# Performance work log

Hardware: AMD Instinct MI355X
Metric: run time of the kernel (lower is better)

The kernel has to match this reference:

```python
import jax, jax.numpy as jnp
import numpy as np

B, T, C = 128, 512, 512
EPS = 1e-5


def setup_inputs() -> dict:
    key = jax.random.key(0)
    ks = jax.random.split(key, 12)
    s_tri = 1.0 / np.sqrt(T)   # rough torch Linear init scale (per-row fan-in varies; fixed for simplicity)
    s_fc1 = 1.0 / np.sqrt(C)
    s_fc2 = 1.0 / np.sqrt(2 * C)
    return {
        "inputs": jax.random.normal(ks[0], (B, T, C), dtype=jnp.float32),
        "ln1_w": jnp.ones((T, C), jnp.float32),
        "ln1_b": jnp.zeros((T, C), jnp.float32),
        "ln2_w": jnp.ones((T, C), jnp.float32),
        "ln2_b": jnp.zeros((T, C), jnp.float32),
        # Row s of triu_W corresponds to nn.Linear(s+1, 1); entries j> s are masked in reference().
        "triu_W": jax.random.uniform(ks[1], (T, T), jnp.float32, -s_tri, s_tri),
        "triu_b": jax.random.uniform(ks[2], (T,), jnp.float32, -s_tri, s_tri),
        "fc1_W": jax.random.uniform(ks[3], (2 * C, C), jnp.float32, -s_fc1, s_fc1),
        "fc1_b": jax.random.uniform(ks[4], (2 * C,), jnp.float32, -s_fc1, s_fc1),
        "fc2_W": jax.random.uniform(ks[5], (C, 2 * C), jnp.float32, -s_fc2, s_fc2),
        "fc2_b": jax.random.uniform(ks[6], (C,), jnp.float32, -s_fc2, s_fc2),
    }


def _layernorm_2d(x, w, b):
    # torch nn.LayerNorm((T, C)): normalize jointly over the last TWO dims.
    mu = jnp.mean(x, axis=(-2, -1), keepdims=True)
    var = jnp.var(x, axis=(-2, -1), keepdims=True)
    return (x - mu) * jax.lax.rsqrt(var + EPS) * w + b


def reference(inputs, ln1_w, ln1_b, ln2_w, ln2_b, triu_W, triu_b, fc1_W, fc1_b, fc2_W, fc2_b):
    x = _layernorm_2d(inputs, ln1_w, ln1_b)                       # [B,T,C]
    # TriU time mixer on x.mT ([B,C,T]): out[..., s] = sum_{t<=s} W[s,t]*x[..., t] + b[s]
    Wm = jnp.tril(triu_W)                                          # causal mask
    xm = jnp.einsum('btc,st->bsc', x, Wm) + triu_b[None, :, None]  # [B,T,C] (already back-transposed)
    x2 = _layernorm_2d(xm + inputs, ln2_w, ln2_b)                  # [B,T,C]
    h = jax.nn.gelu(jnp.einsum('btc,hc->bth', x2, fc1_W) + fc1_b, approximate=False)
    y = jnp.einsum('bth,ch->btc', h, fc2_W) + fc2_b
    return x2 + y
```

## Files before the change

### kernel.cpp

```cpp
#include <hip/hip_runtime.h>
#include <cstdint>

typedef unsigned short u16;
typedef __attribute__((ext_vector_type(8))) short s16x8;
typedef __attribute__((ext_vector_type(4))) float f32x4;
typedef __attribute__((ext_vector_type(8))) unsigned short u16x8;
typedef __attribute__((ext_vector_type(4))) unsigned short u16x4;

#define B_ 128
#define T_ 512
#define C_ 512
#define TC 262144

static __device__ __forceinline__ float bf2f(u16 u) {
  union { unsigned int i; float f; } v; v.i = ((unsigned int)u) << 16; return v.f;
}
static __device__ __forceinline__ u16 f2bf(float f) {
  union { float fv; unsigned int i; } v; v.fv = f;
  unsigned int r = (v.i + 0x7FFFu + ((v.i >> 16) & 1u)) >> 16;
  return (u16)r;
}

static __device__ __forceinline__ float gelu_tanh(float x) {
  float z = 0.7978845608028654f * (x + 0.044715f * x * x * x);
  float e = __expf(2.0f * z);
  float t = 1.0f - 2.0f / (e + 1.0f);
  return 0.5f * x * (1.0f + t);
}

#define GLD16(gp, lp) __builtin_amdgcn_global_load_lds( \
    (const __attribute__((address_space(1))) void*)(gp), \
    (__attribute__((address_space(3))) void*)(lp), 16, 0, 0)


__global__ __launch_bounds__(256)
void reduce_stats_kernel(const float* __restrict__ X, float2* __restrict__ partials) {
  const int b = blockIdx.y, blk = blockIdx.x, tid = threadIdx.x;
  const float* p = X + (size_t)b * TC + (size_t)blk * 2048 + (size_t)tid * 8;
  f32x4 v0 = *(const f32x4*)p;
  f32x4 v1 = *(const f32x4*)(p + 4);
  float s = 0.f, q = 0.f;
#pragma unroll
  for (int i = 0; i < 4; ++i) { s += v0[i] + v1[i]; q += v0[i] * v0[i] + v1[i] * v1[i]; }
  for (int o = 32; o; o >>= 1) { s += __shfl_down(s, o); q += __shfl_down(q, o); }
  __shared__ float ss[4], qq[4];
  if ((tid & 63) == 0) { ss[tid >> 6] = s; qq[tid >> 6] = q; }
  __syncthreads();
  if (tid == 0)
    partials[(size_t)b * 128 + blk] =
        make_float2(ss[0] + ss[1] + ss[2] + ss[3], qq[0] + qq[1] + qq[2] + qq[3]);
}

__global__ __launch_bounds__(128)
void finalize_stats_kernel(const float2* __restrict__ partials, float2* __restrict__ stats) {
  const int b = blockIdx.x, tid = threadIdx.x;
  float2 v = partials[(size_t)b * 128 + tid];
  float s = v.x, q = v.y;
  for (int o = 32; o; o >>= 1) { s += __shfl_down(s, o); q += __shfl_down(q, o); }
  __shared__ float ss[2], qq[2];
  if ((tid & 63) == 0) { ss[tid >> 6] = s; qq[tid >> 6] = q; }
  __syncthreads();
  if (tid == 0) {
    float sm = ss[0] + ss[1], sq = qq[0] + qq[1];
    float mean = sm * (1.f / (float)TC);
    float var = sq * (1.f / (float)TC) - mean * mean;
    stats[b] = make_float2(mean, rsqrtf(var + 1e-5f));
  }
}

__global__ __launch_bounds__(64)
void finalize_stats16_kernel(const float2* __restrict__ partials, float2* __restrict__ stats) {
  const int b = blockIdx.x, tid = threadIdx.x;
  float s = 0.f, q = 0.f;
  if (tid < 16) { float2 v = partials[(size_t)b * 16 + tid]; s = v.x; q = v.y; }
  for (int o = 32; o; o >>= 1) { s += __shfl_down(s, o); q += __shfl_down(q, o); }
  if (tid == 0) {
    float mean = s * (1.f / (float)TC);
    float var = q * (1.f / (float)TC) - mean * mean;
    stats[b] = make_float2(mean, rsqrtf(var + 1e-5f));
  }
}


__global__ __launch_bounds__(256)
void ln1_transpose_kernel(const float* __restrict__ X, const float* __restrict__ W,
                          const float* __restrict__ Bv, const float2* __restrict__ stats,
                          u16* __restrict__ xT) {
  const int b = blockIdx.z;
  const int t0 = blockIdx.y * 64, c0 = blockIdx.x * 64;
  const float2 st = stats[b];
  const float mu = st.x, rs = st.y;
  __shared__ u16 tile[64][72];
  const int tid = threadIdx.x;
  const int rr = tid >> 4;
  const int cc = (tid & 15) * 4;
#pragma unroll
  for (int i = 0; i < 4; ++i) {
    const int lt = i * 16 + rr;
    const size_t wi = (size_t)(t0 + lt) * C_ + c0 + cc;
    f32x4 x = *(const f32x4*)(X + (size_t)b * TC + wi);
    f32x4 w = *(const f32x4*)(W + wi);
    f32x4 bb = *(const f32x4*)(Bv + wi);
#pragma unroll
    for (int j = 0; j < 4; ++j)
      tile[lt][cc + j] = f2bf((x[j] - mu) * rs * w[j] + bb[j]);
  }
  __syncthreads();
  const int c = tid >> 2;
  const int tg = (tid & 3) * 16;
  u16 buf[16];
#pragma unroll
  for (int i = 0; i < 16; ++i) buf[i] = tile[tg + i][c];
  const size_t o = (size_t)b * TC + (size_t)(c0 + c) * T_ + t0 + tg;
  u16x8 o0, o1;
#pragma unroll
  for (int i = 0; i < 8; ++i) { o0[i] = buf[i]; o1[i] = buf[8 + i]; }
  *(u16x8*)(xT + o) = o0;
  *(u16x8*)(xT + o + 8) = o1;
}


__global__ __launch_bounds__(256)
void ln2_apply_kernel(const u16* __restrict__ S, const float* __restrict__ W,
                      const float* __restrict__ Bv, const float2* __restrict__ stats,
                      u16* __restrict__ x2) {
  const size_t i = ((size_t)blockIdx.x * 256 + threadIdx.x) * 8;
  const int b = (int)(i >> 18);
  const size_t r = i & (size_t)(TC - 1);
  const float2 st = stats[b];
  const float mu = st.x, rs = st.y;
  u16x8 sv = *(const u16x8*)(S + i);
  f32x4 w0 = *(const f32x4*)(W + r);
  f32x4 w1 = *(const f32x4*)(W + r + 4);
  f32x4 b0 = *(const f32x4*)(Bv + r);
  f32x4 b1 = *(const f32x4*)(Bv + r + 4);
  u16x8 o;
#pragma unroll
  for (int j = 0; j < 4; ++j) {
    o[j]     = f2bf((bf2f(sv[j])     - mu) * rs * w0[j] + b0[j]);
    o[4 + j] = f2bf((bf2f(sv[4 + j]) - mu) * rs * w1[j] + b1[j]);
  }
  *(u16x8*)(x2 + i) = o;
}


__global__ __launch_bounds__(256)
void cvt_bf16_kernel(const float* __restrict__ X, u16* __restrict__ Y) {
  const size_t i = ((size_t)blockIdx.x * 256 + threadIdx.x) * 4;
  f32x4 v = *(const f32x4*)(X + i);
  u16x4 o;
#pragma unroll
  for (int j = 0; j < 4; ++j) o[j] = f2bf(v[j]);
  *(u16x4*)(Y + i) = o;
}

__global__ __launch_bounds__(256)
void tril_bf16_kernel(const float* __restrict__ Wt, u16* __restrict__ Y) {
  const int i = blockIdx.x * 256 + threadIdx.x;
  const int s = i >> 9, t = i & 511;
  Y[i] = f2bf(t <= s ? Wt[i] : 0.f);
}


template <int MODE>
__global__ __launch_bounds__(256)
void gemm_bt_kernel(const u16* __restrict__ A, const u16* __restrict__ Bm,
                    int K, int lda, int ldb,
                    void* __restrict__ Cp, int ldc,
                    const float* __restrict__ bias,
                    const void* __restrict__ res,
                    long long strideB, long long strideC,
                    float2* __restrict__ stat_part) {
  __shared__ u16 As[2][128 * 32];
  __shared__ u16 Bs[2][128 * 32];
  const int tid = threadIdx.x;

  const int nwg = gridDim.x;
  const int orig = blockIdx.x;
  const int swz = (orig & 7) * (nwg >> 3) + (orig >> 3);
  int bx, by, bz;
  if (MODE == 0) { bz = swz >> 4; by = (swz >> 2) & 3; bx = swz & 3; }
  else if (MODE == 1) { bz = 0; by = swz >> 3; bx = swz & 7; }
  else { bz = 0; by = swz >> 2; bx = swz & 3; }

  const u16* Bp = Bm + (size_t)bz * (size_t)strideB;
  const int m0 = by * 128, n0 = bx * 128;
  int kTiles = K >> 5;
  if (MODE == 0) { const int need = (by + 1) * 4; if (need < kTiles) kTiles = need; }

  const int lane = tid & 63;
  const int wave = tid >> 6;
  const int wm = (wave >> 1) * 64;
  const int wn = (wave & 1) * 64;
  const int lr = lane & 15;
  const int kg = lane >> 4;

  const int srow = tid >> 2;
  const int ske = (tid & 3) * 8;

  f32x4 acc[4][4];
  const f32x4 zero = {0.f, 0.f, 0.f, 0.f};
#pragma unroll
  for (int m = 0; m < 4; ++m)
#pragma unroll
    for (int n = 0; n < 4; ++n) acc[m][n] = zero;

  auto STAGE = [&](int buf, int kt) {
    const int k0 = kt << 5;
#pragma unroll
    for (int i = 0; i < 2; ++i) {
      const int row = i * 64 + srow;
      const int c = i * 256 + tid;
      GLD16(A + (size_t)(m0 + row) * lda + k0 + ske, &As[buf][c * 8]);
      GLD16(Bp + (size_t)(n0 + row) * ldb + k0 + ske, &Bs[buf][c * 8]);
    }
  };

  STAGE(0, 0);
  int cur = 0;
  for (int kt = 0; kt < kTiles; ++kt) {
    __syncthreads();
    if (kt + 1 < kTiles) STAGE(cur ^ 1, kt + 1);
    s16x8 af[4], bf[4];
#pragma unroll
    for (int m = 0; m < 4; ++m) af[m] = *(const s16x8*)&As[cur][(wm + m * 16 + lr) * 32 + kg * 8];
#pragma unroll
    for (int n = 0; n < 4; ++n) bf[n] = *(const s16x8*)&Bs[cur][(wn + n * 16 + lr) * 32 + kg * 8];
#pragma unroll
    for (int m = 0; m < 4; ++m)
#pragma unroll
      for (int n = 0; n < 4; ++n)
        acc[m][n] = __builtin_amdgcn_mfma_f32_16x16x32_bf16(af[m], bf[n], acc[m][n], 0, 0, 0);
    cur ^= 1;
  }

  if (MODE == 0) {
    u16* Cptr = (u16*)Cp + (size_t)bz * (size_t)strideC;
    const float* inp = (const float*)res + (size_t)bz * (size_t)strideC;
    float psum = 0.f, psq = 0.f;
#pragma unroll
    for (int m = 0; m < 4; ++m) {
      const int rb = m0 + wm + m * 16 + kg * 4;
#pragma unroll
      for (int n = 0; n < 4; ++n) {
        const int col = n0 + wn + n * 16 + lr;
#pragma unroll
        for (int j = 0; j < 4; ++j) {
          const size_t idx = (size_t)(rb + j) * ldc + col;
          float v = acc[m][n][j] + inp[idx] + bias[rb + j];
          psum += v; psq += v * v;
          Cptr[idx] = f2bf(v);
        }
      }
    }
    for (int o = 32; o; o >>= 1) { psum += __shfl_down(psum, o); psq += __shfl_down(psq, o); }
    __shared__ float rs_[4], rq_[4];
    if (lane == 0) { rs_[wave] = psum; rq_[wave] = psq; }
    __syncthreads();
    if (tid == 0)
      stat_part[(size_t)bz * 16 + by * 4 + bx] =
          make_float2(rs_[0] + rs_[1] + rs_[2] + rs_[3], rq_[0] + rq_[1] + rq_[2] + rq_[3]);
  } else if (MODE == 1) {
    u16* Cptr = (u16*)Cp;
#pragma unroll
    for (int m = 0; m < 4; ++m) {
      const int rb = m0 + wm + m * 16 + kg * 4;
#pragma unroll
      for (int n = 0; n < 4; ++n) {
        const int col = n0 + wn + n * 16 + lr;
        const float bs = bias[col];
#pragma unroll
        for (int j = 0; j < 4; ++j) {
          float v = acc[m][n][j] + bs;
          Cptr[(size_t)(rb + j) * ldc + col] = f2bf(gelu_tanh(v));
        }
      }
    }
  } else {
    float* Cptr = (float*)Cp;
    const u16* x2p = (const u16*)res;
#pragma unroll
    for (int m = 0; m < 4; ++m) {
      const int rb = m0 + wm + m * 16 + kg * 4;
#pragma unroll
      for (int n = 0; n < 4; ++n) {
        const int col = n0 + wn + n * 16 + lr;
        const float bs = bias[col];
#pragma unroll
        for (int j = 0; j < 4; ++j) {
          const size_t idx = (size_t)(rb + j) * ldc + col;
          Cptr[idx] = acc[m][n][j] + bs + bf2f(x2p[idx]);
        }
      }
    }
  }
}


extern "C" void kernel_launch(void* const* d_in, const int* in_sizes, int n_in,
                              void* d_out, int out_size, void* d_ws, size_t ws_size,
                              hipStream_t stream) {
  const float* inputs = (const float*)d_in[0];
  const float* ln1_w  = (const float*)d_in[1];
  const float* ln1_b  = (const float*)d_in[2];
  const float* ln2_w  = (const float*)d_in[3];
  const float* ln2_b  = (const float*)d_in[4];
  const float* triu_W = (const float*)d_in[5];
  const float* triu_b = (const float*)d_in[6];
  const float* fc1_W  = (const float*)d_in[7];
  const float* fc1_b  = (const float*)d_in[8];
  const float* fc2_W  = (const float*)d_in[9];
  const float* fc2_b  = (const float*)d_in[10];
  float* out = (float*)d_out;
  (void)in_sizes; (void)n_in; (void)out_size; (void)ws_size;

  char* ws = (char*)d_ws;
  size_t off = 0;
  auto carve = [&](size_t bytes) {
    char* p = ws + off;
    off += (bytes + 255) & ~(size_t)255;
    return p;
  };
  u16* s_bf = (u16*)carve((size_t)B_ * T_ * C_ * 2);
  u16* xT   = (u16*)carve((size_t)B_ * T_ * C_ * 2);
  u16* x2   = xT;
  u16* h    = (u16*)carve((size_t)B_ * T_ * 2 * C_ * 2);
  u16* wmb  = (u16*)carve((size_t)T_ * T_ * 2);
  u16* w1b  = (u16*)carve((size_t)2 * C_ * C_ * 2);
  u16* w2b  = (u16*)carve((size_t)C_ * 2 * C_ * 2);
  float2* partials  = (float2*)carve(128 * 128 * sizeof(float2));
  float2* partials2 = (float2*)carve(128 * 16 * sizeof(float2));
  float2* stats1 = (float2*)carve(128 * sizeof(float2));
  float2* stats2 = (float2*)carve(128 * sizeof(float2));

  reduce_stats_kernel<<<dim3(128, 128), 256, 0, stream>>>(inputs, partials);
  finalize_stats_kernel<<<128, 128, 0, stream>>>(partials, stats1);
  ln1_transpose_kernel<<<dim3(8, 8, 128), 256, 0, stream>>>(inputs, ln1_w, ln1_b, stats1, xT);
  tril_bf16_kernel<<<1024, 256, 0, stream>>>(triu_W, wmb);
  cvt_bf16_kernel<<<512, 256, 0, stream>>>(fc1_W, w1b);
  cvt_bf16_kernel<<<512, 256, 0, stream>>>(fc2_W, w2b);
  gemm_bt_kernel<0><<<2048, 256, 0, stream>>>(
      wmb, xT, 512, 512, 512, s_bf, 512, triu_b, inputs, (long long)TC, (long long)TC, partials2);
  finalize_stats16_kernel<<<128, 64, 0, stream>>>(partials2, stats2);
  ln2_apply_kernel<<<16384, 256, 0, stream>>>(s_bf, ln2_w, ln2_b, stats2, x2);
  gemm_bt_kernel<1><<<4096, 256, 0, stream>>>(
      x2, w1b, 512, 512, 512, h, 1024, fc1_b, nullptr, 0, 0, nullptr);
  gemm_bt_kernel<2><<<2048, 256, 0, stream>>>(
      h, w2b, 1024, 1024, 1024, out, 512, fc2_b, x2, 0, 0, nullptr);
}
```

Before: 416.7 us.

## Enlarge GEMM tiles to 256x256x64 with XOR-swizzled LDS and cheaper GELU

All three GEMMs move from 128x128 tiles with K-step 32 on 256 threads to 256x256 tiles with K-step 64 on 512 threads. Each wave now computes a 128x64 sub-tile. The LDS chunk index is XOR-swizzled by row to avoid bank conflicts, and the stats-partials bookkeeping is adjusted to four tiles per batch. The GELU tanh form is rewritten as x*sigmoid(2z) to save a division. The larger tiles are meant to raise data reuse per LDS byte, but they use 128KB of double-buffered LDS per block, so the requested two blocks per CU cannot both fit. That lowers occupancy, and the grid becomes coarser.

```diff
diff --git a/kernel.cpp b/kernel.cpp
--- a/kernel.cpp
+++ b/kernel.cpp
@@ -21,11 +21,10 @@
   return (u16)r;
 }
 
-static __device__ __forceinline__ float gelu_tanh(float x) {
-  float z = 0.7978845608028654f * (x + 0.044715f * x * x * x);
-  float e = __expf(2.0f * z);
-  float t = 1.0f - 2.0f / (e + 1.0f);
-  return 0.5f * x * (1.0f + t);
+static __device__ __forceinline__ float gelu_fast(float x) {
+  float x2 = x * x;
+  float arg = 1.5957691216057308f * x * fmaf(0.044715f, x2, 1.0f);
+  return x / (1.0f + __expf(-arg));
 }
 
 #define GLD16(gp, lp) __builtin_amdgcn_global_load_lds( \
@@ -69,11 +68,11 @@
 }
 
 __global__ __launch_bounds__(64)
-void finalize_stats16_kernel(const float2* __restrict__ partials, float2* __restrict__ stats) {
+void finalize_stats4_kernel(const float2* __restrict__ partials, float2* __restrict__ stats) {
   const int b = blockIdx.x, tid = threadIdx.x;
   float s = 0.f, q = 0.f;
-  if (tid < 16) { float2 v = partials[(size_t)b * 16 + tid]; s = v.x; q = v.y; }
-  for (int o = 32; o; o >>= 1) { s += __shfl_down(s, o); q += __shfl_down(q, o); }
+  if (tid < 4) { float2 v = partials[(size_t)b * 4 + tid]; s = v.x; q = v.y; }
+  for (int o = 2; o; o >>= 1) { s += __shfl_down(s, o); q += __shfl_down(q, o); }
   if (tid == 0) {
     float mean = s * (1.f / (float)TC);
     float var = q * (1.f / (float)TC) - mean * mean;
@@ -163,7 +162,7 @@
 
 
 template <int MODE>
-__global__ __launch_bounds__(256)
+__global__ __launch_bounds__(512, 2)
 void gemm_bt_kernel(const u16* __restrict__ A, const u16* __restrict__ Bm,
                     int K, int lda, int ldb,
                     void* __restrict__ Cp, int ldc,
@@ -171,48 +170,52 @@
                     const void* __restrict__ res,
                     long long strideB, long long strideC,
                     float2* __restrict__ stat_part) {
-  __shared__ u16 As[2][128 * 32];
-  __shared__ u16 Bs[2][128 * 32];
+  __shared__ u16 As[2][256 * 64];
+  __shared__ u16 Bs[2][256 * 64];
   const int tid = threadIdx.x;
 
   const int nwg = gridDim.x;
   const int orig = blockIdx.x;
   const int swz = (orig & 7) * (nwg >> 3) + (orig >> 3);
   int bx, by, bz;
-  if (MODE == 0) { bz = swz >> 4; by = (swz >> 2) & 3; bx = swz & 3; }
-  else if (MODE == 1) { bz = 0; by = swz >> 3; bx = swz & 7; }
-  else { bz = 0; by = swz >> 2; bx = swz & 3; }
+  if (MODE == 0) { bz = swz >> 2; by = (swz >> 1) & 1; bx = swz & 1; }
+  else if (MODE == 1) { bz = 0; by = swz >> 2; bx = swz & 3; }
+  else { bz = 0; by = swz >> 1; bx = swz & 1; }
 
   const u16* Bp = Bm + (size_t)bz * (size_t)strideB;
-  const int m0 = by * 128, n0 = bx * 128;
-  int kTiles = K >> 5;
+  const int m0 = by * 256, n0 = bx * 256;
+  int kTiles = K >> 6;
   if (MODE == 0) { const int need = (by + 1) * 4; if (need < kTiles) kTiles = need; }
 
   const int lane = tid & 63;
   const int wave = tid >> 6;
-  const int wm = (wave >> 1) * 64;
-  const int wn = (wave & 1) * 64;
+  const int wm = (wave >> 2) * 128;
+  const int wn = (wave & 3) * 64;
   const int lr = lane & 15;
   const int kg = lane >> 4;
 
-  const int srow = tid >> 2;
-  const int ske = (tid & 3) * 8;
-
-  f32x4 acc[4][4];
+  f32x4 acc[8][4];
   const f32x4 zero = {0.f, 0.f, 0.f, 0.f};
 #pragma unroll
-  for (int m = 0; m < 4; ++m)
+  for (int m = 0; m < 8; ++m)
 #pragma unroll
     for (int n = 0; n < 4; ++n) acc[m][n] = zero;
 
   auto STAGE = [&](int buf, int kt) {
-    const int k0 = kt << 5;
-#pragma unroll
-    for (int i = 0; i < 2; ++i) {
-      const int row = i * 64 + srow;
-      const int c = i * 256 + tid;
-      GLD16(A + (size_t)(m0 + row) * lda + k0 + ske, &As[buf][c * 8]);
-      GLD16(Bp + (size_t)(n0 + row) * ldb + k0 + ske, &Bs[buf][c * 8]);
+    const int k0 = kt << 6;
+#pragma unroll
+    for (int p = 0; p < 4; ++p) {
+      const int q = p * 512 + tid;
+      const int r = q >> 3;
+      const int kcs = (q & 7) ^ (r & 7);
+      GLD16(A + (size_t)(m0 + r) * lda + k0 + (kcs << 3), &As[buf][q * 8]);
+    }
+#pragma unroll
+    for (int p = 0; p < 4; ++p) {
+      const int q = p * 512 + tid;
+      const int r = q >> 3;
+      const int kcs = (q & 7) ^ (r & 7);
+      GLD16(Bp + (size_t)(n0 + r) * ldb + k0 + (kcs << 3), &Bs[buf][q * 8]);
     }
   };
 
@@ -221,16 +224,27 @@
   for (int kt = 0; kt < kTiles; ++kt) {
     __syncthreads();
     if (kt + 1 < kTiles) STAGE(cur ^ 1, kt + 1);
-    s16x8 af[4], bf[4];
-#pragma unroll
-    for (int m = 0; m < 4; ++m) af[m] = *(const s16x8*)&As[cur][(wm + m * 16 + lr) * 32 + kg * 8];
-#pragma unroll
-    for (int n = 0; n < 4; ++n) bf[n] = *(const s16x8*)&Bs[cur][(wn + n * 16 + lr) * 32 + kg * 8];
-#pragma unroll
-    for (int m = 0; m < 4; ++m)
-#pragma unroll
-      for (int n = 0; n < 4; ++n)
-        acc[m][n] = __builtin_amdgcn_mfma_f32_16x16x32_bf16(af[m], bf[n], acc[m][n], 0, 0, 0);
+#pragma unroll
+    for (int kk = 0; kk < 2; ++kk) {
+      s16x8 af[8], bf4[4];
+#pragma unroll
+      for (int m = 0; m < 8; ++m) {
+        const int row = wm + m * 16 + lr;
+        const int ch = (kk * 4 + kg) ^ (row & 7);
+        af[m] = *(const s16x8*)&As[cur][row * 64 + ch * 8];
+      }
+#pragma unroll
+      for (int n = 0; n < 4; ++n) {
+        const int row = wn + n * 16 + lr;
+        const int ch = (kk * 4 + kg) ^ (row & 7);
+        bf4[n] = *(const s16x8*)&Bs[cur][row * 64 + ch * 8];
+      }
+#pragma unroll
+      for (int m = 0; m < 8; ++m)
+#pragma unroll
+        for (int n = 0; n < 4; ++n)
+          acc[m][n] = __builtin_amdgcn_mfma_f32_16x16x32_bf16(af[m], bf4[n], acc[m][n], 0, 0, 0);
+    }
     cur ^= 1;
   }
 
@@ -239,7 +253,7 @@
     const float* inp = (const float*)res + (size_t)bz * (size_t)strideC;
     float psum = 0.f, psq = 0.f;
 #pragma unroll
-    for (int m = 0; m < 4; ++m) {
+    for (int m = 0; m < 8; ++m) {
       const int rb = m0 + wm + m * 16 + kg * 4;
 #pragma unroll
       for (int n = 0; n < 4; ++n) {
@@ -254,16 +268,19 @@
       }
     }
     for (int o = 32; o; o >>= 1) { psum += __shfl_down(psum, o); psq += __shfl_down(psq, o); }
-    __shared__ float rs_[4], rq_[4];
+    __shared__ float rs_[8], rq_[8];
     if (lane == 0) { rs_[wave] = psum; rq_[wave] = psq; }
     __syncthreads();
-    if (tid == 0)
-      stat_part[(size_t)bz * 16 + by * 4 + bx] =
-          make_float2(rs_[0] + rs_[1] + rs_[2] + rs_[3], rq_[0] + rq_[1] + rq_[2] + rq_[3]);
+    if (tid == 0) {
+      float s = 0.f, q = 0.f;
+#pragma unroll
+      for (int w = 0; w < 8; ++w) { s += rs_[w]; q += rq_[w]; }
+      stat_part[(size_t)bz * 4 + by * 2 + bx] = make_float2(s, q);
+    }
   } else if (MODE == 1) {
     u16* Cptr = (u16*)Cp;
 #pragma unroll
-    for (int m = 0; m < 4; ++m) {
+    for (int m = 0; m < 8; ++m) {
       const int rb = m0 + wm + m * 16 + kg * 4;
 #pragma unroll
       for (int n = 0; n < 4; ++n) {
@@ -272,7 +289,7 @@
 #pragma unroll
         for (int j = 0; j < 4; ++j) {
           float v = acc[m][n][j] + bs;
-          Cptr[(size_t)(rb + j) * ldc + col] = f2bf(gelu_tanh(v));
+          Cptr[(size_t)(rb + j) * ldc + col] = f2bf(gelu_fast(v));
         }
       }
     }
@@ -280,7 +297,7 @@
     float* Cptr = (float*)Cp;
     const u16* x2p = (const u16*)res;
 #pragma unroll
-    for (int m = 0; m < 4; ++m) {
+    for (int m = 0; m < 8; ++m) {
       const int rb = m0 + wm + m * 16 + kg * 4;
 #pragma unroll
       for (int n = 0; n < 4; ++n) {
@@ -329,7 +346,7 @@
   u16* w1b  = (u16*)carve((size_t)2 * C_ * C_ * 2);
   u16* w2b  = (u16*)carve((size_t)C_ * 2 * C_ * 2);
   float2* partials  = (float2*)carve(128 * 128 * sizeof(float2));
-  float2* partials2 = (float2*)carve(128 * 16 * sizeof(float2));
+  float2* partials2 = (float2*)carve(128 * 4 * sizeof(float2));
   float2* stats1 = (float2*)carve(128 * sizeof(float2));
   float2* stats2 = (float2*)carve(128 * sizeof(float2));
 
@@ -339,12 +356,12 @@
   tril_bf16_kernel<<<1024, 256, 0, stream>>>(triu_W, wmb);
   cvt_bf16_kernel<<<512, 256, 0, stream>>>(fc1_W, w1b);
   cvt_bf16_kernel<<<512, 256, 0, stream>>>(fc2_W, w2b);
-  gemm_bt_kernel<0><<<2048, 256, 0, stream>>>(
+  gemm_bt_kernel<0><<<512, 512, 0, stream>>>(
       wmb, xT, 512, 512, 512, s_bf, 512, triu_b, inputs, (long long)TC, (long long)TC, partials2);
-  finalize_stats16_kernel<<<128, 64, 0, stream>>>(partials2, stats2);
+  finalize_stats4_kernel<<<128, 64, 0, stream>>>(partials2, stats2);
   ln2_apply_kernel<<<16384, 256, 0, stream>>>(s_bf, ln2_w, ln2_b, stats2, x2);
-  gemm_bt_kernel<1><<<4096, 256, 0, stream>>>(
+  gemm_bt_kernel<1><<<1024, 512, 0, stream>>>(
       x2, w1b, 512, 512, 512, h, 1024, fc1_b, nullptr, 0, 0, nullptr);
-  gemm_bt_kernel<2><<<2048, 256, 0, stream>>>(
+  gemm_bt_kernel<2><<<512, 512, 0, stream>>>(
       h, w2b, 1024, 1024, 1024, out, 512, fc2_b, x2, 0, 0, nullptr);
 }
```

New measurement: 404.5 us. 2.9% less time.

## Double GEMM K-tile to 64 with XOR-swizzled LDS, simplify GELU

Applied to the files above, without the earlier changes.

Each GEMM stage now loads a 64-wide K tile instead of 32, halving the number of barrier and stage iterations. The LDS layout uses an XOR swizzle on 16-byte chunks to avoid bank conflicts on fragment reads. The tanh-approximate GELU is rewritten in the equivalent sigmoid form with fewer operations, and launch bounds request two blocks per CU. The larger tile doubles LDS use to 64KB per block, which may limit occupancy despite the launch-bounds hint.

```diff
diff --git a/kernel.cpp b/kernel.cpp
--- a/kernel.cpp
+++ b/kernel.cpp
@@ -21,11 +21,10 @@
   return (u16)r;
 }
 
-static __device__ __forceinline__ float gelu_tanh(float x) {
-  float z = 0.7978845608028654f * (x + 0.044715f * x * x * x);
-  float e = __expf(2.0f * z);
-  float t = 1.0f - 2.0f / (e + 1.0f);
-  return 0.5f * x * (1.0f + t);
+static __device__ __forceinline__ float gelu_fast(float x) {
+  float x2 = x * x;
+  float arg = 1.5957691216057308f * x * fmaf(0.044715f, x2, 1.0f);
+  return x / (1.0f + __expf(-arg));
 }
 
 #define GLD16(gp, lp) __builtin_amdgcn_global_load_lds( \
@@ -73,7 +72,7 @@
   const int b = blockIdx.x, tid = threadIdx.x;
   float s = 0.f, q = 0.f;
   if (tid < 16) { float2 v = partials[(size_t)b * 16 + tid]; s = v.x; q = v.y; }
-  for (int o = 32; o; o >>= 1) { s += __shfl_down(s, o); q += __shfl_down(q, o); }
+  for (int o = 8; o; o >>= 1) { s += __shfl_down(s, o); q += __shfl_down(q, o); }
   if (tid == 0) {
     float mean = s * (1.f / (float)TC);
     float var = q * (1.f / (float)TC) - mean * mean;
@@ -163,7 +162,7 @@
 
 
 template <int MODE>
-__global__ __launch_bounds__(256)
+__global__ __launch_bounds__(256, 2)
 void gemm_bt_kernel(const u16* __restrict__ A, const u16* __restrict__ Bm,
                     int K, int lda, int ldb,
                     void* __restrict__ Cp, int ldc,
@@ -171,8 +170,9 @@
                     const void* __restrict__ res,
                     long long strideB, long long strideC,
                     float2* __restrict__ stat_part) {
-  __shared__ u16 As[2][128 * 32];
-  __shared__ u16 Bs[2][128 * 32];
+  __shared__ u16 Asb[2 * 8192];
+  __shared__ u16 Bsb[2 * 8192];
+  __shared__ float rs_[4], rq_[4];
   const int tid = threadIdx.x;
 
   const int nwg = gridDim.x;
@@ -185,8 +185,8 @@
 
   const u16* Bp = Bm + (size_t)bz * (size_t)strideB;
   const int m0 = by * 128, n0 = bx * 128;
-  int kTiles = K >> 5;
-  if (MODE == 0) { const int need = (by + 1) * 4; if (need < kTiles) kTiles = need; }
+  int kTiles = K >> 6;
+  if (MODE == 0) { const int need = (by + 1) * 2; if (need < kTiles) kTiles = need; }
 
   const int lane = tid & 63;
   const int wave = tid >> 6;
@@ -195,9 +195,6 @@
   const int lr = lane & 15;
   const int kg = lane >> 4;
 
-  const int srow = tid >> 2;
-  const int ske = (tid & 3) * 8;
-
   f32x4 acc[4][4];
   const f32x4 zero = {0.f, 0.f, 0.f, 0.f};
 #pragma unroll
@@ -206,13 +203,21 @@
     for (int n = 0; n < 4; ++n) acc[m][n] = zero;
 
   auto STAGE = [&](int buf, int kt) {
-    const int k0 = kt << 5;
-#pragma unroll
-    for (int i = 0; i < 2; ++i) {
-      const int row = i * 64 + srow;
-      const int c = i * 256 + tid;
-      GLD16(A + (size_t)(m0 + row) * lda + k0 + ske, &As[buf][c * 8]);
-      GLD16(Bp + (size_t)(n0 + row) * ldb + k0 + ske, &Bs[buf][c * 8]);
+    const int k0 = kt << 6;
+    const int d = buf * 8192;
+#pragma unroll
+    for (int p = 0; p < 4; ++p) {
+      const int q = p * 256 + tid;
+      const int r = q >> 3;
+      const int kcs = (q & 7) ^ (r & 7);
+      GLD16(A + (size_t)(m0 + r) * lda + k0 + (kcs << 3), &Asb[d + q * 8]);
+    }
+#pragma unroll
+    for (int p = 0; p < 4; ++p) {
+      const int q = p * 256 + tid;
+      const int r = q >> 3;
+      const int kcs = (q & 7) ^ (r & 7);
+      GLD16(Bp + (size_t)(n0 + r) * ldb + k0 + (kcs << 3), &Bsb[d + q * 8]);
     }
   };
 
@@ -221,16 +226,25 @@
   for (int kt = 0; kt < kTiles; ++kt) {
     __syncthreads();
     if (kt + 1 < kTiles) STAGE(cur ^ 1, kt + 1);
-    s16x8 af[4], bf[4];
-#pragma unroll
-    for (int m = 0; m < 4; ++m) af[m] = *(const s16x8*)&As[cur][(wm + m * 16 + lr) * 32 + kg * 8];
-#pragma unroll
-    for (int n = 0; n < 4; ++n) bf[n] = *(const s16x8*)&Bs[cur][(wn + n * 16 + lr) * 32 + kg * 8];
-#pragma unroll
-    for (int m = 0; m < 4; ++m)
-#pragma unroll
-      for (int n = 0; n < 4; ++n)
-        acc[m][n] = __builtin_amdgcn_mfma_f32_16x16x32_bf16(af[m], bf[n], acc[m][n], 0, 0, 0);
+#pragma unroll
+    for (int kk = 0; kk < 2; ++kk) {
+      s16x8 af[4], bfv[4];
+#pragma unroll
+      for (int m = 0; m < 4; ++m) {
+        const int row = wm + m * 16 + lr;
+        af[m] = *(const s16x8*)&Asb[cur * 8192 + row * 64 + (((kk * 4 + kg) ^ (row & 7)) << 3)];
+      }
+#pragma unroll
+      for (int n = 0; n < 4; ++n) {
+        const int row = wn + n * 16 + lr;
+        bfv[n] = *(const s16x8*)&Bsb[cur * 8192 + row * 64 + (((kk * 4 + kg) ^ (row & 7)) << 3)];
+      }
+#pragma unroll
+      for (int m = 0; m < 4; ++m)
+#pragma unroll
+        for (int n = 0; n < 4; ++n)
+          acc[m][n] = __builtin_amdgcn_mfma_f32_16x16x32_bf16(af[m], bfv[n], acc[m][n], 0, 0, 0);
+    }
     cur ^= 1;
   }
 
@@ -254,7 +268,6 @@
       }
     }
     for (int o = 32; o; o >>= 1) { psum += __shfl_down(psum, o); psq += __shfl_down(psq, o); }
-    __shared__ float rs_[4], rq_[4];
     if (lane == 0) { rs_[wave] = psum; rq_[wave] = psq; }
     __syncthreads();
     if (tid == 0)
@@ -272,7 +285,7 @@
 #pragma unroll
         for (int j = 0; j < 4; ++j) {
           float v = acc[m][n][j] + bs;
-          Cptr[(size_t)(rb + j) * ldc + col] = f2bf(gelu_tanh(v));
+          Cptr[(size_t)(rb + j) * ldc + col] = f2bf(gelu_fast(v));
         }
       }
     }
```

After: 387.6 us. 1.08x faster.
